# Kernel tuning notes

Hardware: AMD Instinct MI355X
Metric: run time of the kernel (lower is better)

Reference implementation:

```python
import jax, jax.numpy as jnp
import numpy as np

N = 100000

def _norm_edges(edge_index, n):
    # add self loops, compute symmetric GCN normalization
    loop = jnp.arange(n, dtype=edge_index.dtype)
    src = jnp.concatenate([edge_index[0], loop])
    dst = jnp.concatenate([edge_index[1], loop])
    deg = jax.ops.segment_sum(jnp.ones_like(dst, dtype=jnp.float32), dst, num_segments=n)
    dinv = jnp.where(deg > 0, deg ** -0.5, 0.0)
    norm = dinv[src] * dinv[dst]
    return src, dst, norm

def _gcn(x, W, b, src, dst, norm, n):
    h = x @ W  # [N, out]
    msg = h[src] * norm[:, None]
    return jax.ops.segment_sum(msg, dst, num_segments=n) + b

def setup_inputs() -> dict:
    key = jax.random.key(0)
    ks = jax.random.split(key, 20)
    E = 3200000
    d_in, d_out = 64, 64
    def w(k, i, o):
        return jax.random.normal(k, (i, o), dtype=jnp.float32) * (1.0 / np.sqrt(i))
    return {
        "x": jax.random.normal(ks[0], (N, d_in), dtype=jnp.float32),
        "t": jax.random.normal(ks[1], (N,), dtype=jnp.float32),
        "edge_index": jax.random.randint(ks[2], (2, E), 0, N, dtype=jnp.int64),
        "W1": w(ks[3], d_in + 1, 64), "b1": jnp.zeros((64,), jnp.float32),
        "W2": w(ks[4], 64, 128), "b2": jnp.zeros((128,), jnp.float32),
        "W3": w(ks[5], 128, 256), "b3": jnp.zeros((256,), jnp.float32),
        "W4": w(ks[6], 256, 128), "b4": jnp.zeros((128,), jnp.float32),
        "F1": w(ks[7], 128, 256), "c1": jnp.zeros((256,), jnp.float32),
        "F2": w(ks[8], 256, 128), "c2": jnp.zeros((128,), jnp.float32),
        "F3": w(ks[9], 128, d_out), "c3": jnp.zeros((d_out,), jnp.float32),
    }

def reference(x, t, edge_index, W1, b1, W2, b2, W3, b3, W4, b4, F1, c1, F2, c2, F3, c3):
    n = x.shape[0]
    src, dst, norm = _norm_edges(edge_index, n)
    h = jnp.concatenate([x, t[:, None]], axis=1)
    h = jax.nn.gelu(_gcn(h, W1, b1, src, dst, norm, n))
    h = jax.nn.gelu(_gcn(h, W2, b2, src, dst, norm, n))
    h = jax.nn.gelu(_gcn(h, W3, b3, src, dst, norm, n))
    h = jax.nn.gelu(_gcn(h, W4, b4, src, dst, norm, n))
    h = jax.nn.gelu(h @ F1 + c1)
    h = jax.nn.gelu(h @ F2 + c2)
    return h @ F3 + c3
```

## Files before the change

kernel.cpp:

```cpp
#include <hip/hip_runtime.h>

static constexpr int BLK = 256;

typedef double d2 __attribute__((ext_vector_type(2)));

__device__ __forceinline__ double gelu_d(double v){
  double u = 0.7978845608028654 * (v + 0.044715 * v * v * v);
  return 0.5 * v * (1.0 + tanh(u));
}

__global__ void zero_k(int* __restrict__ a, int n){
  int stride = gridDim.x * blockDim.x;
  for (int i = blockIdx.x*blockDim.x + threadIdx.x; i < n; i += stride) a[i] = 0;
}

__global__ void detect_k(const int* __restrict__ ei, int* __restrict__ flag){
  if (threadIdx.x == 0 && blockIdx.x == 0){
    int zeros = 0;
    for (int i = 0; i < 64; ++i) if (ei[2*i + 1] == 0) ++zeros;
    *flag = (zeros >= 48) ? 1 : 0;
  }
}

__global__ void count_k(const int* __restrict__ ei, int E, const int* __restrict__ flag,
                        int* __restrict__ cnt){
  int is64 = *flag;
  int stride = gridDim.x * blockDim.x;
  for (int e = blockIdx.x*blockDim.x + threadIdx.x; e < E; e += stride){
    int d = is64 ? ei[2*(E + e)] : ei[E + e];
    atomicAdd(&cnt[d], 1);
  }
}

__global__ void dinv_k(const int* __restrict__ cnt, double* __restrict__ dinv, int n){
  int i = blockIdx.x*blockDim.x + threadIdx.x;
  if (i < n){
    double deg = (double)(cnt[i] + 1);
    dinv[i] = 1.0 / sqrt(deg);
  }
}

__global__ __launch_bounds__(256)
void scanA_k(const int* __restrict__ cnt, int* __restrict__ partial, int n, int chunk){
  __shared__ int red[256];
  int b = blockIdx.x;
  int lo = b * chunk, hi = min(n, lo + chunk);
  int s = 0;
  for (int i = lo + threadIdx.x; i < hi; i += 256) s += cnt[i];
  red[threadIdx.x] = s; __syncthreads();
  for (int off = 128; off > 0; off >>= 1){
    if (threadIdx.x < off) red[threadIdx.x] += red[threadIdx.x + off];
    __syncthreads();
  }
  if (threadIdx.x == 0) partial[b] = red[0];
}

__global__ __launch_bounds__(256)
void scanB_k(int* __restrict__ partial, int nb){
  __shared__ int sd[256];
  int tid = threadIdx.x;
  int v = (tid < nb) ? partial[tid] : 0;
  sd[tid] = v; __syncthreads();
  for (int off = 1; off < 256; off <<= 1){
    int t = (tid >= off) ? sd[tid - off] : 0;
    __syncthreads();
    sd[tid] += t;
    __syncthreads();
  }
  if (tid < nb) partial[tid] = sd[tid] - v;
  if (tid == 255) partial[nb] = sd[255];
}

__global__ __launch_bounds__(256)
void scanC_k(const int* __restrict__ cnt, const int* __restrict__ partial,
             int* __restrict__ rp, int n, int chunk, int nb){
  __shared__ int sd[256];
  int b = blockIdx.x;
  int lo = b * chunk, hi = min(n, lo + chunk);
  int run = partial[b];
  for (int base = lo; base < hi; base += 256){
    int i = base + threadIdx.x;
    int v = (i < hi) ? cnt[i] : 0;
    sd[threadIdx.x] = v; __syncthreads();
    for (int off = 1; off < 256; off <<= 1){
      int t = (threadIdx.x >= off) ? sd[threadIdx.x - off] : 0;
      __syncthreads();
      sd[threadIdx.x] += t;
      __syncthreads();
    }
    if (i < hi) rp[i] = run + sd[threadIdx.x] - v;
    run += sd[255];
    __syncthreads();
  }
  if (b == 0 && threadIdx.x == 0) rp[n] = partial[nb];
}

__global__ void scatter_k(const int* __restrict__ ei, int E, const int* __restrict__ flag,
                          const int* __restrict__ rp, int* __restrict__ fill,
                          const double* __restrict__ dinv,
                          int* __restrict__ col, double* __restrict__ val){
  int is64 = *flag;
  int stride = gridDim.x * blockDim.x;
  for (int e = blockIdx.x*blockDim.x + threadIdx.x; e < E; e += stride){
    int s = is64 ? ei[2*e]       : ei[e];
    int d = is64 ? ei[2*(E + e)] : ei[E + e];
    int p = rp[d] + atomicAdd(&fill[d], 1);
    col[p] = s;
    if (val) val[p] = dinv[s];
  }
}

template<typename ST>
__global__ void concat_k(const float* __restrict__ x, const float* __restrict__ t,
                         ST* __restrict__ h0, int n){
  int total = n * 66;
  int stride = gridDim.x * blockDim.x;
  for (int idx = blockIdx.x*blockDim.x + threadIdx.x; idx < total; idx += stride){
    int row = idx / 66;
    int c = idx - row * 66;
    float v = (c < 64) ? x[row*64 + c] : (c == 64 ? t[row] : 0.0f);
    h0[idx] = (ST)v;
  }
}

template<typename ST>
__global__ __launch_bounds__(256, 2)
void gemm_k(const ST* __restrict__ A, int K, int lda,
            const float* __restrict__ W, int NOUT,
            const float* __restrict__ bias,
            ST* __restrict__ C, float* __restrict__ Cf,
            int n, int fuse)
{
  __shared__ __align__(16) double As[128][34];
  __shared__ __align__(16) double Ws[32][66];
  int row0 = blockIdx.x * 128;
  int col0 = blockIdx.y * 64;
  int tid = threadIdx.x;
  int tr = tid >> 4, tc = tid & 15;
  int c0 = 2 * tc;
  double acc[8][4] = {};
  int ktiles = (K + 31) / 32;
  for (int kt = 0; kt < ktiles; ++kt){
    int k0 = kt * 32;
    {
      int r  = tid >> 1;
      int kk = (tid & 1) * 16;
      int gr = row0 + r;
      const ST* Ap = A + (size_t)gr * lda + k0 + kk;
      #pragma unroll
      for (int u = 0; u < 16; ++u){
        int kg = k0 + kk + u;
        As[r][kk + u] = (gr < n && kg < K) ? (double)Ap[u] : 0.0;
      }
    }
    {
      int r = tid >> 3;
      int c = (tid & 7) * 8;
      int kg = k0 + r;
      const float* Wp = W + (size_t)kg * NOUT + col0 + c;
      #pragma unroll
      for (int u = 0; u < 8; ++u)
        Ws[r][c + u] = (kg < K) ? (double)Wp[u] : 0.0;
    }
    __syncthreads();
    #pragma unroll
    for (int kk = 0; kk < 32; kk += 2){
      d2 w0a = *(const d2*)&Ws[kk    ][c0];
      d2 w0b = *(const d2*)&Ws[kk    ][c0 + 32];
      d2 w1a = *(const d2*)&Ws[kk + 1][c0];
      d2 w1b = *(const d2*)&Ws[kk + 1][c0 + 32];
      #pragma unroll
      for (int i = 0; i < 8; ++i){
        d2 av = *(const d2*)&As[tr + 16*i][kk];
        acc[i][0] = fma(av.x, w0a.x, acc[i][0]);
        acc[i][1] = fma(av.x, w0a.y, acc[i][1]);
        acc[i][2] = fma(av.x, w0b.x, acc[i][2]);
        acc[i][3] = fma(av.x, w0b.y, acc[i][3]);
        acc[i][0] = fma(av.y, w1a.x, acc[i][0]);
        acc[i][1] = fma(av.y, w1a.y, acc[i][1]);
        acc[i][2] = fma(av.y, w1b.x, acc[i][2]);
        acc[i][3] = fma(av.y, w1b.y, acc[i][3]);
      }
    }
    __syncthreads();
  }
  #pragma unroll
  for (int i = 0; i < 8; ++i){
    int r = row0 + tr + 16*i;
    if (r >= n) continue;
    #pragma unroll
    for (int j = 0; j < 4; ++j){
      int c = col0 + ((j < 2) ? (c0 + j) : (c0 + 30 + j));
      double v = acc[i][j];
      if (fuse){ v += (double)bias[c]; if (fuse == 1) v = gelu_d(v); }
      if (fuse == 2) __builtin_nontemporal_store((float)v, &Cf[(size_t)r * NOUT + c]);
      else           __builtin_nontemporal_store((ST)v,   &C [(size_t)r * NOUT + c]);
    }
  }
}

template<typename ST, int NC>
__global__ __launch_bounds__(256)
void agg_k(const ST* __restrict__ T, const int* __restrict__ rp,
           const int* __restrict__ col, const double* __restrict__ val,
           const double* __restrict__ dinv, const float* __restrict__ bias,
           ST* __restrict__ O, int n, int fuse)
{
  constexpr int DOUT = NC * 64;
  int w = (blockIdx.x * blockDim.x + threadIdx.x) >> 6;
  int lane = threadIdx.x & 63;
  if (w >= n) return;
  double dv = dinv[w];
  const ST* Ti = T + (size_t)w * DOUT;
  double acc[NC];
  #pragma unroll
  for (int c = 0; c < NC; ++c) acc[c] = dv * (double)Ti[lane + 64*c];
  int e  = rp[w];
  int e1 = rp[w + 1];
  if (val){
    for (; e + 4 <= e1; e += 4){
      int s0 = __builtin_nontemporal_load(&col[e]);
      int s1 = __builtin_nontemporal_load(&col[e+1]);
      int s2 = __builtin_nontemporal_load(&col[e+2]);
      int s3 = __builtin_nontemporal_load(&col[e+3]);
      double v0 = __builtin_nontemporal_load(&val[e]);
      double v1 = __builtin_nontemporal_load(&val[e+1]);
      double v2 = __builtin_nontemporal_load(&val[e+2]);
      double v3 = __builtin_nontemporal_load(&val[e+3]);
      const ST* T0 = T + (size_t)s0 * DOUT;
      const ST* T1 = T + (size_t)s1 * DOUT;
      const ST* T2 = T + (size_t)s2 * DOUT;
      const ST* T3 = T + (size_t)s3 * DOUT;
      double t0[NC], t1[NC], t2[NC], t3[NC];
      #pragma unroll
      for (int c = 0; c < NC; ++c){
        t0[c] = (double)T0[lane + 64*c];
        t1[c] = (double)T1[lane + 64*c];
        t2[c] = (double)T2[lane + 64*c];
        t3[c] = (double)T3[lane + 64*c];
      }
      #pragma unroll
      for (int c = 0; c < NC; ++c){
        acc[c] = fma(v0, t0[c], acc[c]);
        acc[c] = fma(v1, t1[c], acc[c]);
        acc[c] = fma(v2, t2[c], acc[c]);
        acc[c] = fma(v3, t3[c], acc[c]);
      }
    }
    for (; e < e1; ++e){
      int s = __builtin_nontemporal_load(&col[e]);
      double v = __builtin_nontemporal_load(&val[e]);
      const ST* Ts = T + (size_t)s * DOUT;
      #pragma unroll
      for (int c = 0; c < NC; ++c) acc[c] = fma(v, (double)Ts[lane + 64*c], acc[c]);
    }
  } else {
    for (; e < e1; ++e){
      int s = col[e];
      double v = dinv[s];
      const ST* Ts = T + (size_t)s * DOUT;
      #pragma unroll
      for (int c = 0; c < NC; ++c) acc[c] = fma(v, (double)Ts[lane + 64*c], acc[c]);
    }
  }
  ST* Oi = O + (size_t)w * DOUT;
  #pragma unroll
  for (int c = 0; c < NC; ++c){
    double v = dv * acc[c];
    if (fuse) v = gelu_d(v + (double)bias[lane + 64*c]);
    __builtin_nontemporal_store((ST)v, &Oi[lane + 64*c]);
  }
}

template<typename ST>
static void run_net(const float* x, const float* t,
                    const float* W1, const float* b1, const float* W2, const float* b2,
                    const float* W3, const float* b3, const float* W4, const float* b4,
                    const float* F1, const float* c1, const float* F2, const float* c2,
                    const float* F3, const float* c3,
                    ST* b256, ST* ba, ST* bb,
                    const int* rp, const int* col, const double* val, const double* dinv,
                    float* out, int N, hipStream_t stream)
{
  auto gemm = [&](const ST* A, int K, int lda, const float* W, int NOUT, const float* bias,
                  ST* C, float* Cf, int fuse){
    dim3 g((N + 127) / 128, NOUT / 64);
    gemm_k<ST><<<g, dim3(BLK), 0, stream>>>(A, K, lda, W, NOUT, bias, C, Cf, N, fuse);
  };
  int aggGrid = (N * 64 + BLK - 1) / BLK;
  auto agg64 = [&](const ST* T, const float* bias, ST* O, int fuse){
    agg_k<ST,1><<<dim3(aggGrid), dim3(BLK), 0, stream>>>(T, rp, col, val, dinv, bias, O, N, fuse);
  };
  auto agg128 = [&](const ST* T, const float* bias, ST* O, int fuse){
    agg_k<ST,2><<<dim3(aggGrid), dim3(BLK), 0, stream>>>(T, rp, col, val, dinv, bias, O, N, fuse);
  };

  concat_k<ST><<<dim3(1024), dim3(BLK), 0, stream>>>(x, t, ba, N);
  gemm(ba, 65, 66, W1, 64, nullptr, bb, nullptr, 0);
  agg64(bb, b1, ba, 1);
  agg64(ba, nullptr, bb, 0);
  gemm(bb, 64, 64, W2, 128, b2, ba, nullptr, 1);
  agg128(ba, nullptr, bb, 0);
  gemm(bb, 128, 128, W3, 256, b3, b256, nullptr, 1);
  gemm(b256, 256, 256, W4, 128, nullptr, ba, nullptr, 0);
  agg128(ba, b4, bb, 1);
  gemm(bb, 128, 128, F1, 256, c1, b256, nullptr, 1);
  gemm(b256, 256, 256, F2, 128, c2, ba, nullptr, 1);
  gemm(ba, 128, 128, F3, 64, c3, nullptr, out, 2);
}

extern "C" void kernel_launch(void* const* d_in, const int* in_sizes, int n_in,
                              void* d_out, int out_size, void* d_ws, size_t ws_size,
                              hipStream_t stream)
{
  const float* x  = (const float*)d_in[0];
  const float* t  = (const float*)d_in[1];
  const int*   ei = (const int*)d_in[2];
  const float* W1 = (const float*)d_in[3];  const float* b1 = (const float*)d_in[4];
  const float* W2 = (const float*)d_in[5];  const float* b2 = (const float*)d_in[6];
  const float* W3 = (const float*)d_in[7];  const float* b3 = (const float*)d_in[8];
  const float* W4 = (const float*)d_in[9];  const float* b4 = (const float*)d_in[10];
  const float* F1 = (const float*)d_in[11]; const float* c1 = (const float*)d_in[12];
  const float* F2 = (const float*)d_in[13]; const float* c2 = (const float*)d_in[14];
  const float* F3 = (const float*)d_in[15]; const float* c3 = (const float*)d_in[16];
  float* out = (float*)d_out;
  int N = in_sizes[0] / 64;
  int E = in_sizes[2] / 2;

  char* p = (char*)d_ws;
  auto alloc = [&](size_t b){ char* r = p; p += (b + 255) & ~(size_t)255; return (void*)r; };
  int*    flag    = (int*)alloc(4);
  int*    cnt     = (int*)alloc((size_t)N * 4);
  int*    fill    = (int*)alloc((size_t)N * 4);
  int*    rp      = (int*)alloc((size_t)(N + 1) * 4);
  int*    partial = (int*)alloc((size_t)257 * 4);
  int*    col     = (int*)alloc((size_t)E * 4);
  double* dinv    = (double*)alloc((size_t)N * 8);
  size_t base = (size_t)(p - (char*)d_ws);

  size_t actElems = (size_t)N * 512;
  size_t valBytes = ((size_t)E * 8 + 255) & ~(size_t)255;
  bool f64val = ws_size >= base + valBytes + actElems * sizeof(double);
  bool f64ok  = f64val || ws_size >= base + actElems * sizeof(double);
  bool f32val = ws_size >= base + valBytes + actElems * sizeof(float);
  bool f32ok  = f32val || ws_size >= base + actElems * sizeof(float);
  if (!f32ok) return;

  double* val = nullptr;
  if ((f64ok && f64val) || (!f64ok && f32val)) val = (double*)alloc((size_t)E * 8);

  int nb = 256;
  int chunk = (N + nb - 1) / nb;
  zero_k<<<dim3(256), dim3(BLK), 0, stream>>>(cnt, N);
  zero_k<<<dim3(256), dim3(BLK), 0, stream>>>(fill, N);
  detect_k<<<1, 64, 0, stream>>>(ei, flag);
  count_k<<<dim3(4096), dim3(BLK), 0, stream>>>(ei, E, flag, cnt);
  dinv_k<<<dim3((N + BLK - 1) / BLK), dim3(BLK), 0, stream>>>(cnt, dinv, N);
  scanA_k<<<dim3(nb), dim3(256), 0, stream>>>(cnt, partial, N, chunk);
  scanB_k<<<dim3(1), dim3(256), 0, stream>>>(partial, nb);
  scanC_k<<<dim3(nb), dim3(256), 0, stream>>>(cnt, partial, rp, N, chunk, nb);
  scatter_k<<<dim3(4096), dim3(BLK), 0, stream>>>(ei, E, flag, rp, fill, dinv, col, val);

  if (f64ok){
    double* b256 = (double*)alloc((size_t)N * 256 * 8);
    double* ba   = (double*)alloc((size_t)N * 128 * 8);
    double* bb   = (double*)alloc((size_t)N * 128 * 8);
    run_net<double>(x, t, W1, b1, W2, b2, W3, b3, W4, b4, F1, c1, F2, c2, F3, c3,
                    b256, ba, bb, rp, col, val, dinv, out, N, stream);
  } else {
    float* b256 = (float*)alloc((size_t)N * 256 * 4);
    float* ba   = (float*)alloc((size_t)N * 128 * 4);
    float* bb   = (float*)alloc((size_t)N * 128 * 4);
    run_net<float>(x, t, W1, b1, W2, b2, W3, b3, W4, b4, F1, c1, F2, c2, F3, c3,
                   b256, ba, bb, rp, col, val, dinv, out, N, stream);
  }
}
```

Baseline: 2.553 ms.

## Prefetch next GEMM tile into registers and widen column tile for wide outputs

The FP64 GEMM now loads the next K-tile of A and W into registers while the current tile is being computed, a register-level double buffer that hides global load latency. It is also templated on the column-tile width, so outputs with 128 or more columns use 128-wide tiles and each block reuses its loaded A tile across more columns. The A loads drop the per-element K bound check, so rows may be read past the end of the buffer. Slack bytes are added to the activation allocations to keep those reads in bounds. The wider tile raises register pressure, which may lower occupancy.

```diff
diff --git a/kernel.cpp b/kernel.cpp
--- a/kernel.cpp
+++ b/kernel.cpp
@@ -123,7 +123,7 @@
   }
 }
 
-template<typename ST>
+template<typename ST, int CT>
 __global__ __launch_bounds__(256, 2)
 void gemm_k(const ST* __restrict__ A, int K, int lda,
             const float* __restrict__ W, int NOUT,
@@ -131,55 +131,81 @@
             ST* __restrict__ C, float* __restrict__ Cf,
             int n, int fuse)
 {
+  constexpr int TW  = 16 * CT;
+  constexpr int WPT = TW / 8;
   __shared__ __align__(16) double As[128][34];
-  __shared__ __align__(16) double Ws[32][66];
+  __shared__ __align__(16) double Ws[32][TW + 2];
   int row0 = blockIdx.x * 128;
-  int col0 = blockIdx.y * 64;
+  int col0 = blockIdx.y * TW;
   int tid = threadIdx.x;
   int tr = tid >> 4, tc = tid & 15;
   int c0 = 2 * tc;
-  double acc[8][4] = {};
+  double acc[8][CT] = {};
+
+  int sar = tid >> 1;
+  int sak = (tid & 1) * 16;
+  int swr = tid >> 3;
+  int swc = (tid & 7) * WPT;
+
   int ktiles = (K + 31) / 32;
+
+  double ga[16];
+  float  gw[WPT];
+  {
+    int gr = row0 + sar;
+    const ST* Ap = A + (size_t)gr * lda + sak;
+    bool rok = (gr < n);
+    #pragma unroll
+    for (int u = 0; u < 16; ++u) ga[u] = rok ? (double)Ap[u] : 0.0;
+    const float* Wp = W + (size_t)swr * NOUT + col0 + swc;
+    bool wok = (swr < K);
+    #pragma unroll
+    for (int u = 0; u < WPT; ++u) gw[u] = wok ? Wp[u] : 0.0f;
+  }
+
   for (int kt = 0; kt < ktiles; ++kt){
-    int k0 = kt * 32;
-    {
-      int r  = tid >> 1;
-      int kk = (tid & 1) * 16;
-      int gr = row0 + r;
-      const ST* Ap = A + (size_t)gr * lda + k0 + kk;
-      #pragma unroll
-      for (int u = 0; u < 16; ++u){
-        int kg = k0 + kk + u;
-        As[r][kk + u] = (gr < n && kg < K) ? (double)Ap[u] : 0.0;
+    #pragma unroll
+    for (int g = 0; g < 8; ++g){
+      d2 v; v.x = ga[2*g]; v.y = ga[2*g+1];
+      *(d2*)&As[sar][sak + 2*g] = v;
+    }
+    #pragma unroll
+    for (int g = 0; g < WPT/2; ++g){
+      d2 v; v.x = (double)gw[2*g]; v.y = (double)gw[2*g+1];
+      *(d2*)&Ws[swr][swc + 2*g] = v;
+    }
+    __syncthreads();
+    if (kt + 1 < ktiles){
+      int k0 = (kt + 1) * 32;
+      int gr = row0 + sar;
+      const ST* Ap = A + (size_t)gr * lda + k0 + sak;
+      bool rok = (gr < n);
+      #pragma unroll
+      for (int u = 0; u < 16; ++u) ga[u] = rok ? (double)Ap[u] : 0.0;
+      int kg = k0 + swr;
+      const float* Wp = W + (size_t)kg * NOUT + col0 + swc;
+      bool wok = (kg < K);
+      #pragma unroll
+      for (int u = 0; u < WPT; ++u) gw[u] = wok ? Wp[u] : 0.0f;
+    }
+    #pragma unroll
+    for (int kk = 0; kk < 32; kk += 2){
+      d2 w0[CT/2], w1[CT/2];
+      #pragma unroll
+      for (int q = 0; q < CT/2; ++q){
+        w0[q] = *(const d2*)&Ws[kk    ][c0 + 32*q];
+        w1[q] = *(const d2*)&Ws[kk + 1][c0 + 32*q];
       }
-    }
-    {
-      int r = tid >> 3;
-      int c = (tid & 7) * 8;
-      int kg = k0 + r;
-      const float* Wp = W + (size_t)kg * NOUT + col0 + c;
-      #pragma unroll
-      for (int u = 0; u < 8; ++u)
-        Ws[r][c + u] = (kg < K) ? (double)Wp[u] : 0.0;
-    }
-    __syncthreads();
-    #pragma unroll
-    for (int kk = 0; kk < 32; kk += 2){
-      d2 w0a = *(const d2*)&Ws[kk    ][c0];
-      d2 w0b = *(const d2*)&Ws[kk    ][c0 + 32];
-      d2 w1a = *(const d2*)&Ws[kk + 1][c0];
-      d2 w1b = *(const d2*)&Ws[kk + 1][c0 + 32];
       #pragma unroll
       for (int i = 0; i < 8; ++i){
         d2 av = *(const d2*)&As[tr + 16*i][kk];
-        acc[i][0] = fma(av.x, w0a.x, acc[i][0]);
-        acc[i][1] = fma(av.x, w0a.y, acc[i][1]);
-        acc[i][2] = fma(av.x, w0b.x, acc[i][2]);
-        acc[i][3] = fma(av.x, w0b.y, acc[i][3]);
-        acc[i][0] = fma(av.y, w1a.x, acc[i][0]);
-        acc[i][1] = fma(av.y, w1a.y, acc[i][1]);
-        acc[i][2] = fma(av.y, w1b.x, acc[i][2]);
-        acc[i][3] = fma(av.y, w1b.y, acc[i][3]);
+        #pragma unroll
+        for (int q = 0; q < CT/2; ++q){
+          acc[i][2*q  ] = fma(av.x, w0[q].x, acc[i][2*q  ]);
+          acc[i][2*q+1] = fma(av.x, w0[q].y, acc[i][2*q+1]);
+          acc[i][2*q  ] = fma(av.y, w1[q].x, acc[i][2*q  ]);
+          acc[i][2*q+1] = fma(av.y, w1[q].y, acc[i][2*q+1]);
+        }
       }
     }
     __syncthreads();
@@ -189,8 +215,8 @@
     int r = row0 + tr + 16*i;
     if (r >= n) continue;
     #pragma unroll
-    for (int j = 0; j < 4; ++j){
-      int c = col0 + ((j < 2) ? (c0 + j) : (c0 + 30 + j));
+    for (int j = 0; j < CT; ++j){
+      int c = col0 + c0 + 32*(j >> 1) + (j & 1);
       double v = acc[i][j];
       if (fuse){ v += (double)bias[c]; if (fuse == 1) v = gelu_d(v); }
       if (fuse == 2) __builtin_nontemporal_store((float)v, &Cf[(size_t)r * NOUT + c]);
@@ -284,8 +310,13 @@
 {
   auto gemm = [&](const ST* A, int K, int lda, const float* W, int NOUT, const float* bias,
                   ST* C, float* Cf, int fuse){
-    dim3 g((N + 127) / 128, NOUT / 64);
-    gemm_k<ST><<<g, dim3(BLK), 0, stream>>>(A, K, lda, W, NOUT, bias, C, Cf, N, fuse);
+    if (NOUT >= 128){
+      dim3 g((N + 127) / 128, NOUT / 128);
+      gemm_k<ST,8><<<g, dim3(BLK), 0, stream>>>(A, K, lda, W, NOUT, bias, C, Cf, N, fuse);
+    } else {
+      dim3 g((N + 127) / 128, NOUT / 64);
+      gemm_k<ST,4><<<g, dim3(BLK), 0, stream>>>(A, K, lda, W, NOUT, bias, C, Cf, N, fuse);
+    }
   };
   int aggGrid = (N * 64 + BLK - 1) / BLK;
   auto agg64 = [&](const ST* T, const float* bias, ST* O, int fuse){
@@ -338,12 +369,13 @@
   double* dinv    = (double*)alloc((size_t)N * 8);
   size_t base = (size_t)(p - (char*)d_ws);
 
+  size_t slackB = 1024;
   size_t actElems = (size_t)N * 512;
   size_t valBytes = ((size_t)E * 8 + 255) & ~(size_t)255;
-  bool f64val = ws_size >= base + valBytes + actElems * sizeof(double);
-  bool f64ok  = f64val || ws_size >= base + actElems * sizeof(double);
-  bool f32val = ws_size >= base + valBytes + actElems * sizeof(float);
-  bool f32ok  = f32val || ws_size >= base + actElems * sizeof(float);
+  bool f64val = ws_size >= base + valBytes + actElems * sizeof(double) + 3*slackB;
+  bool f64ok  = f64val || ws_size >= base + actElems * sizeof(double) + 3*slackB;
+  bool f32val = ws_size >= base + valBytes + actElems * sizeof(float) + 3*slackB;
+  bool f32ok  = f32val || ws_size >= base + actElems * sizeof(float) + 3*slackB;
   if (!f32ok) return;
 
   double* val = nullptr;
@@ -362,15 +394,15 @@
   scatter_k<<<dim3(4096), dim3(BLK), 0, stream>>>(ei, E, flag, rp, fill, dinv, col, val);
 
   if (f64ok){
-    double* b256 = (double*)alloc((size_t)N * 256 * 8);
-    double* ba   = (double*)alloc((size_t)N * 128 * 8);
-    double* bb   = (double*)alloc((size_t)N * 128 * 8);
+    double* b256 = (double*)alloc((size_t)N * 256 * 8 + slackB);
+    double* ba   = (double*)alloc((size_t)N * 128 * 8 + slackB);
+    double* bb   = (double*)alloc((size_t)N * 128 * 8 + slackB);
     run_net<double>(x, t, W1, b1, W2, b2, W3, b3, W4, b4, F1, c1, F2, c2, F3, c3,
                     b256, ba, bb, rp, col, val, dinv, out, N, stream);
   } else {
-    float* b256 = (float*)alloc((size_t)N * 256 * 4);
-    float* ba   = (float*)alloc((size_t)N * 128 * 4);
-    float* bb   = (float*)alloc((size_t)N * 128 * 4);
+    float* b256 = (float*)alloc((size_t)N * 256 * 4 + slackB);
+    float* ba   = (float*)alloc((size_t)N * 128 * 4 + slackB);
+    float* bb   = (float*)alloc((size_t)N * 128 * 4 + slackB);
     run_net<float>(x, t, W1, b1, W2, b2, W3, b3, W4, b4, F1, c1, F2, c2, F3, c3,
                    b256, ba, bb, rp, col, val, dinv, out, N, stream);
   }
```

Measured after the change: 2.779 ms. 8.9% more time.
